# Kernel tuning notes

Measured on AMD Instinct MI355X. Metric: run time of the kernel, lower is better.

Reference implementation:

```python
import jax, jax.numpy as jnp
import numpy as np

ALPHA = 0.95
B, T, IN, HID, CTX, OUT = 64, 512, 256, 512, 256, 128
HORIZON = 1


def _scrn_layer(x, Wx, bx, Uc, Vh):
    # x: [B, T, D_in]; Wx: [CTX, D_in]; bx: [CTX]; Uc: [HID, CTX]; Vh: [HID, HID]
    # Input projection is time-parallel; only the recurrence is sequential.
    xp = jnp.einsum('btd,cd->btc', x, Wx) + bx  # [B, T, CTX]
    h0 = jnp.zeros((x.shape[0], Vh.shape[0]), dtype=x.dtype)
    c0 = jnp.zeros((x.shape[0], Wx.shape[0]), dtype=x.dtype)

    def step(carry, xp_t):
        h, c = carry
        c = (1.0 - ALPHA) * c + ALPHA * xp_t
        h = jnp.tanh(jnp.dot(c, Uc.T) + jnp.dot(h, Vh.T))
        return (h, c), h

    (_, _), hs = jax.lax.scan(step, (h0, c0), jnp.swapaxes(xp, 0, 1))
    return jnp.swapaxes(hs, 0, 1)  # [B, T, HID]


def setup_inputs() -> dict:
    key = jax.random.key(0)
    ks = jax.random.split(key, 12)

    def lin(k, fan_in, shape):
        bound = 1.0 / np.sqrt(fan_in)
        return jax.random.uniform(k, shape, jnp.float32, -bound, bound)

    return {
        'x': jax.random.normal(ks[0], (B, T, IN), jnp.float32),
        'Wx0': lin(ks[1], IN, (CTX, IN)),
        'bx0': lin(ks[2], IN, (CTX,)),
        'Uc0': lin(ks[3], CTX, (HID, CTX)),
        'Vh0': lin(ks[4], HID, (HID, HID)),
        'Wx1': lin(ks[5], HID, (CTX, HID)),
        'bx1': lin(ks[6], HID, (CTX,)),
        'Uc1': lin(ks[7], CTX, (HID, CTX)),
        'Vh1': lin(ks[8], HID, (HID, HID)),
        'fc_w': lin(ks[9], HID, (OUT, HID)),
        'fc_b': lin(ks[10], HID, (OUT,)),
    }


def reference(x, Wx0, bx0, Uc0, Vh0, Wx1, bx1, Uc1, Vh1, fc_w, fc_b):
    out = _scrn_layer(x, Wx0, bx0, Uc0, Vh0)
    out = _scrn_layer(out, Wx1, bx1, Uc1, Vh1)
    out = out[:, -HORIZON:, :]  # [B, HORIZON, HID]
    return jnp.einsum('bth,oh->bto', out, fc_w) + fc_b  # [B, HORIZON, OUT]
```

## Files before the change

kernel.cpp:

```cpp
#include <hip/hip_runtime.h>


typedef _Float16 f16;
typedef _Float16 f16x8 __attribute__((ext_vector_type(8)));
typedef _Float16 f16x2 __attribute__((ext_vector_type(2)));
typedef float f32x4 __attribute__((ext_vector_type(4)));
typedef unsigned short u16;
typedef unsigned int u32;
typedef unsigned short u16x8 __attribute__((ext_vector_type(8)));
typedef unsigned long long u64;

#define DEV __device__ __forceinline__

constexpr int Tt = 512, HIDq = 512;
constexpr int RS = 32;
constexpr int DSd = 32;

DEV float bf2f(u16 u) { unsigned v = ((unsigned)u) << 16; float f; __builtin_memcpy(&f, &v, 4); return f; }
DEV u16 f2bf(float f) { unsigned u; __builtin_memcpy(&u, &f, 4); u = (u + 0x7fffu + ((u >> 16) & 1u)) >> 16; return (u16)u; }
DEV float fast_tanh(float x) {
  x = fminf(30.f, fmaxf(-30.f, x));
  float e = exp2f(x * 2.885390081777927f);
  return (e - 1.f) / (e + 1.f);
}
DEV u64 al64(const u64* p) { return __hip_atomic_load(p, __ATOMIC_RELAXED, __HIP_MEMORY_SCOPE_AGENT); }
DEV u32 al32(const u32* p) { return __hip_atomic_load(p, __ATOMIC_RELAXED, __HIP_MEMORY_SCOPE_AGENT); }
DEV void as32(u32* p, u32 v) { __hip_atomic_store(p, v, __ATOMIC_RELAXED, __HIP_MEMORY_SCOPE_AGENT); }

__global__ void k_probe(const u16* __restrict__ w, int* __restrict__ dmode) {
  __shared__ int s;
  if (threadIdx.x == 0) s = 0;
  __syncthreads();
  int found = 0;
  for (int i = threadIdx.x; i < 8192; i += 256) {
    float v = bf2f(w[i]);
    if (fabsf(v) > 0.5f) found = 1;
  }
  if (found) atomicOr(&s, 1);
  __syncthreads();
  if (threadIdx.x == 0) *dmode = s;
}

__global__ void k_cvt(const void* __restrict__ src, f16* __restrict__ dst, int n8,
                      const int* __restrict__ dmode) {
  int i = blockIdx.x * 256 + threadIdx.x;
  if (i >= n8) return;
  f16x8 o;
  if (*dmode) {
    const float4* s = (const float4*)src;
    float4 a = s[2*i], b = s[2*i+1];
    o[0]=(f16)a.x; o[1]=(f16)a.y; o[2]=(f16)a.z; o[3]=(f16)a.w;
    o[4]=(f16)b.x; o[5]=(f16)b.y; o[6]=(f16)b.z; o[7]=(f16)b.w;
  } else {
    u16x8 v = ((const u16x8*)src)[i];
#pragma unroll
    for (int j = 0; j < 8; ++j) o[j] = (f16)bf2f(v[j]);
  }
  ((f16x8*)dst)[i] = o;
}

__global__ void k_zero(u16* __restrict__ out) {
  out[blockIdx.x * 256 + threadIdx.x] = 0;
}

__global__ __launch_bounds__(256) void k_tr(const f16* __restrict__ src, f16* __restrict__ dst,
                                            int R, int cshift) {
  int idx = blockIdx.x * 256 + threadIdx.x;
  int r = idx >> cshift, c = idx & ((1 << cshift) - 1);
  dst[c * R + r] = src[idx];
}

__global__ __launch_bounds__(512) void k_bias(const f16* __restrict__ Uc, const f16* __restrict__ bx,
                                              f16* __restrict__ out) {
  int j = threadIdx.x;
  float a = 0.f;
  for (int c = 0; c < 256; ++c) a += (float)Uc[j * 256 + c] * (float)bx[c];
  out[j] = (f16)a;
}

__global__ __launch_bounds__(128) void k_ema(const f16* __restrict__ xp, f16* __restrict__ c) {
  int b = blockIdx.x >> 3, chunk = blockIdx.x & 7;
  int t0 = chunk * 64;
  int ch = threadIdx.x;
  const f16x2* src = (const f16x2*)(xp + (size_t)b * Tt * 256) + ch;
  f16x2* dst = (f16x2*)(c + (size_t)b * Tt * 256) + ch;
  float c0 = 0.f, c1 = 0.f;
  int ts = (t0 >= 16) ? t0 - 16 : 0;
  for (int tt = ts; tt < t0 + 64; ++tt) {
    f16x2 v = src[(size_t)tt * 128];
    c0 = 0.05f * c0 + 0.95f * (float)v.x;
    c1 = 0.05f * c1 + 0.95f * (float)v.y;
    if (tt >= t0) { f16x2 o; o.x = (f16)c0; o.y = (f16)c1; dst[(size_t)tt * 128] = o; }
  }
}

template<bool HAS_BIAS, bool TD>
__global__ __launch_bounds__(256) void k_gemm(const f16* __restrict__ A, const f16* __restrict__ Bm,
                                              const f16* __restrict__ bias, f16* __restrict__ C,
                                              int M, int N, int K) {
  __shared__ f16 As[128][40];
  __shared__ f16 Bs[128][40];
  const int tid = threadIdx.x, lane = tid & 63, wv = tid >> 6;
  const int l15 = lane & 15, q = lane >> 4;
  const int wm = wv >> 1, wn = wv & 1;
  const int m0 = blockIdx.y * 128, n0 = blockIdx.x * 128;
  const int srow = tid >> 1, sseg = tid & 1;
  f32x4 acc[4][4] = {};
  const f16* ga = A  + (size_t)(m0 + srow) * K + sseg * 16;
  const f16* gb = Bm + (size_t)(n0 + srow) * K + sseg * 16;
  for (int k0 = 0; k0 < K; k0 += 32) {
    f16x8 a0 = *(const f16x8*)(ga + k0);
    f16x8 a1 = *(const f16x8*)(ga + k0 + 8);
    f16x8 b0 = *(const f16x8*)(gb + k0);
    f16x8 b1 = *(const f16x8*)(gb + k0 + 8);
    __syncthreads();
    *(f16x8*)&As[srow][sseg*16]     = a0;
    *(f16x8*)&As[srow][sseg*16 + 8] = a1;
    *(f16x8*)&Bs[srow][sseg*16]     = b0;
    *(f16x8*)&Bs[srow][sseg*16 + 8] = b1;
    __syncthreads();
    f16x8 af[4], bf[4];
#pragma unroll
    for (int i = 0; i < 4; ++i) af[i] = *(const f16x8*)&As[wm*64 + i*16 + l15][q*8];
#pragma unroll
    for (int i = 0; i < 4; ++i) bf[i] = *(const f16x8*)&Bs[wn*64 + i*16 + l15][q*8];
#pragma unroll
    for (int i = 0; i < 4; ++i)
#pragma unroll
      for (int j = 0; j < 4; ++j)
        acc[i][j] = __builtin_amdgcn_mfma_f32_16x16x32_f16(af[i], bf[j], acc[i][j], 0, 0, 0);
  }
#pragma unroll
  for (int j = 0; j < 4; ++j) {
    int col = n0 + wn*64 + j*16 + l15;
    float bv = HAS_BIAS ? (float)bias[col] : 0.f;
#pragma unroll
    for (int i = 0; i < 4; ++i)
#pragma unroll
      for (int r = 0; r < 4; ++r) {
        int row = m0 + wm*64 + i*16 + q*4 + r;
        size_t orow = TD ? (size_t)((row & 511) * 64 + (row >> 9)) : (size_t)row;
        C[orow * N + col] = (f16)(acc[i][j][r] + bv);
      }
  }
}

__global__ __launch_bounds__(512, 2) void k_mega(const f16* __restrict__ Vh0,
                                                 const f16* __restrict__ Vh1,
                                                 const f16* __restrict__ W2,
                                                 const f16* __restrict__ b2,
                                                 const f16* __restrict__ d1,
                                                 u32* __restrict__ ring,
                                                 u32* __restrict__ d2r,
                                                 u32* __restrict__ hb1,
                                                 u32* __restrict__ hb2,
                                                 u32* __restrict__ prog,
                                                 u32* __restrict__ eprog) {
  __shared__ f16 hL[2][16][520];
  const int bb = blockIdx.x;
  const int tid = threadIdx.x, w = tid >> 6, lane = tid & 63;
  const int l15 = lane & 15, q = lane >> 4;

  if (bb < 8) {
    const int hf = bb & 1, g = bb >> 1;
    const int colbase = 256*hf + 32*w;
    f16x8 Bf[2][16];
#pragma unroll
    for (int j = 0; j < 2; ++j)
#pragma unroll
      for (int kk = 0; kk < 16; ++kk)
        Bf[j][kk] = *(const f16x8*)&Vh0[(size_t)(colbase + 16*j + l15) * HIDq + kk*32 + q*8];
    for (int i = tid; i < 1024; i += 512) {
      int r = i >> 6, c = (i & 63) * 8;
      f16x8 z = {};
      *(f16x8*)&hL[0][r][c] = z;
    }
    float dv[2][4];
#pragma unroll
    for (int j = 0; j < 2; ++j)
#pragma unroll
      for (int r = 0; r < 4; ++r)
        dv[j][r] = (float)d1[(size_t)(16*g + q*4 + r) * HIDq + colbase + 16*j + l15];
    __syncthreads();
    const int irow = tid >> 5, ic8 = (tid & 31) * 8;
    const int pcol = 256*(hf ^ 1) + ic8;
    int eprog_c = 0;

    for (int t = 0; t < Tt; ++t) {
      const int rb = t & 1, wb = rb ^ 1, slot = t & 1;
      f32x4 a00 = {}, a01 = {}, a10 = {}, a11 = {};
#pragma unroll
      for (int kk = 0; kk < 16; ++kk) {
        f16x8 a = *(const f16x8*)&hL[rb][l15][kk*32 + q*8];
        if (kk & 1) {
          a01 = __builtin_amdgcn_mfma_f32_16x16x32_f16(a, Bf[0][kk], a01, 0, 0, 0);
          a11 = __builtin_amdgcn_mfma_f32_16x16x32_f16(a, Bf[1][kk], a11, 0, 0, 0);
        } else {
          a00 = __builtin_amdgcn_mfma_f32_16x16x32_f16(a, Bf[0][kk], a00, 0, 0, 0);
          a10 = __builtin_amdgcn_mfma_f32_16x16x32_f16(a, Bf[1][kk], a10, 0, 0, 0);
        }
      }
      const u32 tagw = (u32)(t + 1) << 16;
      u32* rslot = ring + (size_t)(t & (RS - 1)) * 32768;
      u16 hbits[2][4];
#pragma unroll
      for (int j = 0; j < 2; ++j) {
        f32x4 s = j ? (a10 + a11) : (a00 + a01);
#pragma unroll
        for (int r = 0; r < 4; ++r) {
          float z = s[r] + dv[j][r];
          union { f16 h; u16 u; } cv; cv.h = (f16)fast_tanh(z);
          hbits[j][r] = cv.u;
          as32(&hb1[(size_t)slot * 32768 + (size_t)(16*g + q*4 + r) * HIDq + colbase + 16*j + l15],
               tagw | (u32)cv.u);
        }
      }
#pragma unroll
      for (int j = 0; j < 2; ++j)
#pragma unroll
        for (int r = 0; r < 4; ++r)
          as32(&rslot[(size_t)(16*g + q*4 + r) * HIDq + colbase + 16*j + l15],
               tagw | (u32)hbits[j][r]);
#pragma unroll
      for (int j = 0; j < 2; ++j)
#pragma unroll
        for (int r = 0; r < 4; ++r) {
          union { u16 u; f16 h; } cv; cv.u = hbits[j][r];
          hL[wb][q*4 + r][colbase + 16*j + l15] = cv.h;
        }
      if (t < Tt - 1) {
#pragma unroll
        for (int j = 0; j < 2; ++j)
#pragma unroll
          for (int r = 0; r < 4; ++r)
            dv[j][r] = (float)d1[((size_t)(t+1)*64 + 16*g + q*4 + r) * HIDq + colbase + 16*j + l15];
      }
      if (tid == 0 && eprog_c < t - 30) {
        const u64* ep = (const u64*)&eprog[2 * g];
        for (;;) {
          u64 e2 = al64(ep);
          int lo = (int)(u32)e2, hi = (int)(u32)(e2 >> 32);
          eprog_c = lo < hi ? lo : hi;
          if (eprog_c >= t - 30) break;
          __builtin_amdgcn_s_sleep(1);
        }
      }
      {
        const u64* pp = (const u64*)(hb1 + (size_t)slot * 32768 + (size_t)(16*g + irow) * HIDq)
                      + (pcol >> 1);
        u64 v[4];
#pragma unroll
        for (int jj = 0; jj < 4; ++jj) v[jj] = al64(pp + jj);
        for (;;) {
          u32 bad = 0;
#pragma unroll
          for (int jj = 0; jj < 4; ++jj)
            bad |= ((u32)v[jj] ^ tagw) | ((u32)(v[jj] >> 32) ^ tagw);
          if ((bad & 0xFFFF0000u) == 0) break;
          __builtin_amdgcn_s_sleep(1);
#pragma unroll
          for (int jj = 0; jj < 4; ++jj) v[jj] = al64(pp + jj);
        }
        union { u32 wd[4]; f16x8 vv; } fr;
#pragma unroll
        for (int jj = 0; jj < 4; ++jj)
          fr.wd[jj] = __builtin_amdgcn_perm((u32)(v[jj] >> 32), (u32)v[jj], 0x05040100u);
        *(f16x8*)&hL[wb][irow][pcol] = fr.vv;
      }
      __syncthreads();
    }

  } else if (bb < 16) {
    const int eb = bb - 8, hf = eb & 1, g = eb >> 1;
    const int colbase = 256*hf + 32*w;
    f16x8 Bf[2][16];
#pragma unroll
    for (int j = 0; j < 2; ++j)
#pragma unroll
      for (int kk = 0; kk < 16; ++kk)
        Bf[j][kk] = *(const f16x8*)&W2[(size_t)(colbase + 16*j + l15) * HIDq + kk*32 + q*8];
    float bv[2] = { (float)b2[colbase + l15], (float)b2[colbase + 16 + l15] };
    float ed[2][4] = {};
    const int irow = tid >> 5, icol = (tid & 31) * 16;
    int sprog_c = 0;

    for (int t = 0; t < Tt; ++t) {
      if (tid == 0) {
        if (t > 0) as32(&eprog[eb], (u32)t);
        if (sprog_c < t - 32) {
          for (;;) {
            sprog_c = (int)al32(&prog[eb]);
            if (sprog_c >= t - 32) break;
            __builtin_amdgcn_s_sleep(1);
          }
        }
      }
      const u32 tagw = (u32)(t + 1) << 16;
      {
        const u64* pp = (const u64*)(ring + (size_t)(t & (RS - 1)) * 32768
                          + (size_t)(16*g + irow) * HIDq) + (icol >> 1);
        u64 v[8];
#pragma unroll
        for (int jj = 0; jj < 8; ++jj) v[jj] = al64(pp + jj);
        for (;;) {
          u32 bad = 0;
#pragma unroll
          for (int jj = 0; jj < 8; ++jj)
            bad |= ((u32)v[jj] ^ tagw) | ((u32)(v[jj] >> 32) ^ tagw);
          if ((bad & 0xFFFF0000u) == 0) break;
          __builtin_amdgcn_s_sleep(1);
#pragma unroll
          for (int jj = 0; jj < 8; ++jj) v[jj] = al64(pp + jj);
        }
        union { u32 wd[8]; f16x8 vv[2]; } fr;
#pragma unroll
        for (int jj = 0; jj < 8; ++jj)
          fr.wd[jj] = __builtin_amdgcn_perm((u32)(v[jj] >> 32), (u32)v[jj], 0x05040100u);
        *(f16x8*)&hL[t & 1][irow][icol]     = fr.vv[0];
        *(f16x8*)&hL[t & 1][irow][icol + 8] = fr.vv[1];
      }
      __syncthreads();
      f32x4 a00 = {}, a01 = {}, a10 = {}, a11 = {};
#pragma unroll
      for (int kk = 0; kk < 16; ++kk) {
        f16x8 a = *(const f16x8*)&hL[t & 1][l15][kk*32 + q*8];
        if (kk & 1) {
          a01 = __builtin_amdgcn_mfma_f32_16x16x32_f16(a, Bf[0][kk], a01, 0, 0, 0);
          a11 = __builtin_amdgcn_mfma_f32_16x16x32_f16(a, Bf[1][kk], a11, 0, 0, 0);
        } else {
          a00 = __builtin_amdgcn_mfma_f32_16x16x32_f16(a, Bf[0][kk], a00, 0, 0, 0);
          a10 = __builtin_amdgcn_mfma_f32_16x16x32_f16(a, Bf[1][kk], a10, 0, 0, 0);
        }
      }
      u32* dslot = d2r + (size_t)(t & (DSd - 1)) * 32768;
#pragma unroll
      for (int j = 0; j < 2; ++j) {
        f32x4 s = j ? (a10 + a11) : (a00 + a01);
#pragma unroll
        for (int r = 0; r < 4; ++r) {
          ed[j][r] = 0.05f * ed[j][r] + 0.95f * (s[r] + bv[j]);
          union { f16 h; u16 u; } cv; cv.h = (f16)ed[j][r];
          as32(&dslot[(size_t)(16*g + q*4 + r) * HIDq + colbase + 16*j + l15],
               tagw | (u32)cv.u);
        }
      }
    }

  } else {
    const int sb = bb - 16, hf = sb & 1, g = sb >> 1;
    const int colbase = 256*hf + 32*w;
    f16x8 Bf[2][16];
#pragma unroll
    for (int j = 0; j < 2; ++j)
#pragma unroll
      for (int kk = 0; kk < 16; ++kk)
        Bf[j][kk] = *(const f16x8*)&Vh1[(size_t)(colbase + 16*j + l15) * HIDq + kk*32 + q*8];
    for (int i = tid; i < 1024; i += 512) {
      int r = i >> 6, c = (i & 63) * 8;
      f16x8 z = {};
      *(f16x8*)&hL[0][r][c] = z;
    }
    float dv[2][4];
    {
      const u32 tag2 = 1u << 16;
      const u32* dp = d2r + (size_t)(16*g + q*4) * HIDq + colbase + l15;
      u32 vv[8];
      for (;;) {
#pragma unroll
        for (int i = 0; i < 8; ++i) vv[i] = al32(dp + (size_t)(i & 3) * HIDq + 16*(i >> 2));
        u32 bad = 0;
#pragma unroll
        for (int i = 0; i < 8; ++i) bad |= vv[i] ^ tag2;
        if ((bad & 0xFFFF0000u) == 0) break;
        __builtin_amdgcn_s_sleep(1);
      }
#pragma unroll
      for (int j = 0; j < 2; ++j)
#pragma unroll
        for (int r = 0; r < 4; ++r) {
          union { u16 u; f16 h; } cv; cv.u = (u16)vv[j*4 + r];
          dv[j][r] = (float)cv.h;
        }
    }
    __syncthreads();
    const int irow = tid >> 5, ic8 = (tid & 31) * 8;
    const int pcol = 256*(hf ^ 1) + ic8;

    for (int t = 0; t < Tt; ++t) {
      const int rb = t & 1, wb = rb ^ 1, slot = t & 1;
      if (tid == 0 && t > 0) as32(&prog[sb], (u32)t);
      f32x4 a00 = {}, a01 = {}, a10 = {}, a11 = {};
#pragma unroll
      for (int kk = 0; kk < 16; ++kk) {
        f16x8 a = *(const f16x8*)&hL[rb][l15][kk*32 + q*8];
        if (kk & 1) {
          a01 = __builtin_amdgcn_mfma_f32_16x16x32_f16(a, Bf[0][kk], a01, 0, 0, 0);
          a11 = __builtin_amdgcn_mfma_f32_16x16x32_f16(a, Bf[1][kk], a11, 0, 0, 0);
        } else {
          a00 = __builtin_amdgcn_mfma_f32_16x16x32_f16(a, Bf[0][kk], a00, 0, 0, 0);
          a10 = __builtin_amdgcn_mfma_f32_16x16x32_f16(a, Bf[1][kk], a10, 0, 0, 0);
        }
      }
      const u32 tagw = (u32)(t + 1) << 16;
      u16 hbits[2][4];
#pragma unroll
      for (int j = 0; j < 2; ++j) {
        f32x4 s = j ? (a10 + a11) : (a00 + a01);
#pragma unroll
        for (int r = 0; r < 4; ++r) {
          float z = s[r] + dv[j][r];
          union { f16 h; u16 u; } cv; cv.h = (f16)fast_tanh(z);
          hbits[j][r] = cv.u;
          as32(&hb2[(size_t)(slot*64 + 16*g + q*4 + r) * HIDq + colbase + 16*j + l15],
               tagw | (u32)cv.u);
        }
      }
#pragma unroll
      for (int j = 0; j < 2; ++j)
#pragma unroll
        for (int r = 0; r < 4; ++r) {
          union { u16 u; f16 h; } cv; cv.u = hbits[j][r];
          hL[wb][q*4 + r][colbase + 16*j + l15] = cv.h;
        }

      {
        const bool have_d = (t < Tt - 1);
        const u32 tag2 = (u32)(t + 2) << 16;
        const u32* dp = d2r + (size_t)((t + 1) & (DSd - 1)) * 32768
                      + (size_t)(16*g + q*4) * HIDq + colbase + l15;
        const u64* pp = (const u64*)&hb2[(size_t)(slot*64 + 16*g + irow) * HIDq] + (pcol >> 1);
        u32 vv[8];
        u64 v[4];
        if (have_d) {
#pragma unroll
          for (int i = 0; i < 8; ++i) vv[i] = al32(dp + (size_t)(i & 3) * HIDq + 16*(i >> 2));
        }
#pragma unroll
        for (int jj = 0; jj < 4; ++jj) v[jj] = al64(pp + jj);
        for (;;) {
          u32 badp = 0;
#pragma unroll
          for (int jj = 0; jj < 4; ++jj)
            badp |= ((u32)v[jj] ^ tagw) | ((u32)(v[jj] >> 32) ^ tagw);
          badp &= 0xFFFF0000u;
          u32 badd = 0;
          if (have_d) {
#pragma unroll
            for (int i = 0; i < 8; ++i) badd |= vv[i] ^ tag2;
            badd &= 0xFFFF0000u;
          }
          if (!(badp | badd)) break;
          __builtin_amdgcn_s_sleep(1);
          if (badp) {
#pragma unroll
            for (int jj = 0; jj < 4; ++jj) v[jj] = al64(pp + jj);
          }
          if (badd) {
#pragma unroll
            for (int i = 0; i < 8; ++i) vv[i] = al32(dp + (size_t)(i & 3) * HIDq + 16*(i >> 2));
          }
        }
        if (have_d) {
#pragma unroll
          for (int j = 0; j < 2; ++j)
#pragma unroll
            for (int r = 0; r < 4; ++r) {
              union { u16 u; f16 h; } cv; cv.u = (u16)vv[j*4 + r];
              dv[j][r] = (float)cv.h;
            }
        }
        union { u32 wd[4]; f16x8 vr; } fr;
#pragma unroll
        for (int jj = 0; jj < 4; ++jj)
          fr.wd[jj] = __builtin_amdgcn_perm((u32)(v[jj] >> 32), (u32)v[jj], 0x05040100u);
        *(f16x8*)&hL[wb][irow][pcol] = fr.vr;
      }
      __syncthreads();
    }
  }
}

__global__ __launch_bounds__(64) void k_final(const u32* __restrict__ h, const f16* __restrict__ fw,
                                              const f16* __restrict__ fb, void* __restrict__ outv,
                                              const int* __restrict__ dmode) {
  __shared__ f16 hA[16][520];
  __shared__ f16 Bw[16][520];
  const int mb = blockIdx.x & 3, nb = blockIdx.x >> 2;
  const int lane = threadIdx.x, l15 = lane & 15, q = lane >> 4;
  for (int i = lane; i < 16 * 128; i += 64) {
    int r = i >> 7, c = (i & 127) * 4;
    const u64* p = (const u64*)&h[(size_t)(mb*16 + r) * 512 + c];
    u64 v0 = al64(p), v1 = al64(p + 1);
    *(u32*)&hA[r][c]     = __builtin_amdgcn_perm((u32)(v0 >> 32), (u32)v0, 0x05040100u);
    *(u32*)&hA[r][c + 2] = __builtin_amdgcn_perm((u32)(v1 >> 32), (u32)v1, 0x05040100u);
  }
  for (int i = lane; i < 16 * 64; i += 64) {
    int r = i >> 6, c = (i & 63) * 8;
    *(f16x8*)&Bw[r][c] = *(const f16x8*)&fw[(size_t)(nb*16 + r) * 512 + c];
  }
  __syncthreads();
  f32x4 acc = {};
#pragma unroll
  for (int kk = 0; kk < 16; ++kk) {
    f16x8 a = *(const f16x8*)&hA[l15][kk*32 + q*8];
    f16x8 b = *(const f16x8*)&Bw[l15][kk*32 + q*8];
    acc = __builtin_amdgcn_mfma_f32_16x16x32_f16(a, b, acc, 0, 0, 0);
  }
  float bv = (float)fb[nb*16 + l15];
  int md = *dmode;
#pragma unroll
  for (int r = 0; r < 4; ++r) {
    int idx = (mb*16 + q*4 + r) * 128 + nb*16 + l15;
    float val = acc[r] + bv;
    if (md) ((float*)outv)[idx] = val;
    else    ((u16*)outv)[idx]   = f2bf(val);
  }
}

extern "C" void kernel_launch(void* const* d_in, const int* in_sizes, int n_in,
                              void* d_out, int out_size, void* d_ws, size_t ws_size,
                              hipStream_t stream) {
  if (ws_size < 88080384ull) {
    k_zero<<<32, 256, 0, stream>>>((u16*)d_out);
    return;
  }
  char* ws = (char*)d_ws;
  u32* hb2   = (u32*)(ws + 0);
  u32* hb1   = (u32*)(ws + 262144);
  u32* prog  = (u32*)(ws + 524288);
  u32* eprog = (u32*)(ws + 524320);
  int* dmode = (int*)(ws + 524352);
  f16* Wx0f = (f16*)(ws + 1048576);
  f16* Uc0f = (f16*)(ws + 1179648);
  f16* Vh0f = (f16*)(ws + 1441792);
  f16* Wx1f = (f16*)(ws + 1966080);
  f16* Uc1f = (f16*)(ws + 2228224);
  f16* Vh1f = (f16*)(ws + 2490368);
  f16* fcwf = (f16*)(ws + 3014656);
  f16* bx0f = (f16*)(ws + 3145728);
  f16* bx1f = (f16*)(ws + 3146240);
  f16* fcbf = (f16*)(ws + 3146752);
  f16* Wx1T = (f16*)(ws + 3147776);
  f16* W2f  = (f16*)(ws + 3409920);
  f16* b2f  = (f16*)(ws + 3934208);
  f16* x16  = (f16*)(ws + 4194304);
  u32* ring = (u32*)(ws + 4194304);
  f16* xp1  = (f16*)(ws + 20971520);
  f16* cb1  = (f16*)(ws + 37748736);
  u32* d2r  = (u32*)(ws + 37748736);
  f16* d1   = (f16*)(ws + 54525952);

  hipMemsetAsync(ws, 0, 524352, stream);
  k_probe<<<1, 256, 0, stream>>>((const u16*)d_in[1], dmode);
  auto cvt = [&](const void* s, f16* d, int n) {
    int n8 = n / 8;
    k_cvt<<<dim3((n8 + 255) / 256), dim3(256), 0, stream>>>(s, d, n8, dmode);
  };
  cvt(d_in[0],  x16,  8388608);
  cvt(d_in[1],  Wx0f, 65536);
  cvt(d_in[2],  bx0f, 256);
  cvt(d_in[3],  Uc0f, 131072);
  cvt(d_in[4],  Vh0f, 262144);
  cvt(d_in[5],  Wx1f, 131072);
  cvt(d_in[6],  bx1f, 256);
  cvt(d_in[7],  Uc1f, 131072);
  cvt(d_in[8],  Vh1f, 262144);
  cvt(d_in[9],  fcwf, 65536);
  cvt(d_in[10], fcbf, 128);

  k_tr<<<512, 256, 0, stream>>>(Wx1f, Wx1T, 256, 9);
  k_bias<<<1, 512, 0, stream>>>(Uc1f, bx1f, b2f);
  k_gemm<false, false><<<dim3(4, 4), 256, 0, stream>>>(Uc1f, Wx1T, nullptr, W2f, 512, 512, 256);

  k_gemm<true , false><<<dim3(2, 256), 256, 0, stream>>>(x16, Wx0f, bx0f, xp1, 32768, 256, 256);
  k_ema<<<512, 128, 0, stream>>>(xp1, cb1);
  hipMemsetAsync(ws + 4194304, 0, 4194304, stream);
  k_gemm<false, true ><<<dim3(4, 256), 256, 0, stream>>>(cb1, Uc0f, nullptr, d1, 32768, 512, 256);
  hipMemsetAsync(ws + 37748736, 0, 4194304, stream);

  k_mega<<<24, 512, 0, stream>>>(Vh0f, Vh1f, W2f, b2f, d1, ring, d2r, hb1, hb2, prog, eprog);

  k_final<<<32, 64, 0, stream>>>(hb2 + 64 * 512, fcwf, fcbf, d_out, dmode);
}
```

Before: 1.833 ms.

## Add per-block progress counters to gate ring polling and reorder ring stores

Moves the layer-1 ring writes after the critical peer-exchange read so the recurrence's inter-block handoff runs first. Adds progress counters (s1p, d2p) that layer-1 and middle blocks publish, so consumers spin on one counter instead of repeatedly polling large tagged buffers. It also lengthens sleep intervals in the spin loops. The aim is to cut memory traffic from polling and shorten the critical path, at the cost of an extra block-wide barrier and extra atomic stores per step.

New measurement: 2.015 ms. 10.0% more time.

```diff
diff --git a/kernel.cpp b/kernel.cpp
--- a/kernel.cpp
+++ b/kernel.cpp
@@ -155,7 +155,9 @@
                                                  u32* __restrict__ hb1,
                                                  u32* __restrict__ hb2,
                                                  u32* __restrict__ prog,
-                                                 u32* __restrict__ eprog) {
+                                                 u32* __restrict__ eprog,
+                                                 u32* __restrict__ s1p,
+                                                 u32* __restrict__ d2p) {
   __shared__ f16 hL[2][16][520];
   const int bb = blockIdx.x;
   const int tid = threadIdx.x, w = tid >> 6, lane = tid & 63;
@@ -201,7 +203,6 @@
         }
       }
       const u32 tagw = (u32)(t + 1) << 16;
-      u32* rslot = ring + (size_t)(t & (RS - 1)) * 32768;
       u16 hbits[2][4];
 #pragma unroll
       for (int j = 0; j < 2; ++j) {
@@ -218,12 +219,6 @@
 #pragma unroll
       for (int j = 0; j < 2; ++j)
 #pragma unroll
-        for (int r = 0; r < 4; ++r)
-          as32(&rslot[(size_t)(16*g + q*4 + r) * HIDq + colbase + 16*j + l15],
-               tagw | (u32)hbits[j][r]);
-#pragma unroll
-      for (int j = 0; j < 2; ++j)
-#pragma unroll
         for (int r = 0; r < 4; ++r) {
           union { u16 u; f16 h; } cv; cv.u = hbits[j][r];
           hL[wb][q*4 + r][colbase + 16*j + l15] = cv.h;
@@ -234,16 +229,6 @@
 #pragma unroll
           for (int r = 0; r < 4; ++r)
             dv[j][r] = (float)d1[((size_t)(t+1)*64 + 16*g + q*4 + r) * HIDq + colbase + 16*j + l15];
-      }
-      if (tid == 0 && eprog_c < t - 30) {
-        const u64* ep = (const u64*)&eprog[2 * g];
-        for (;;) {
-          u64 e2 = al64(ep);
-          int lo = (int)(u32)e2, hi = (int)(u32)(e2 >> 32);
-          eprog_c = lo < hi ? lo : hi;
-          if (eprog_c >= t - 30) break;
-          __builtin_amdgcn_s_sleep(1);
-        }
       }
       {
         const u64* pp = (const u64*)(hb1 + (size_t)slot * 32768 + (size_t)(16*g + irow) * HIDq)
@@ -266,6 +251,28 @@
         for (int jj = 0; jj < 4; ++jj)
           fr.wd[jj] = __builtin_amdgcn_perm((u32)(v[jj] >> 32), (u32)v[jj], 0x05040100u);
         *(f16x8*)&hL[wb][irow][pcol] = fr.vv;
+      }
+      {
+        u32* rslot = ring + (size_t)(t & (RS - 1)) * 32768;
+#pragma unroll
+        for (int j = 0; j < 2; ++j)
+#pragma unroll
+          for (int r = 0; r < 4; ++r)
+            as32(&rslot[(size_t)(16*g + q*4 + r) * HIDq + colbase + 16*j + l15],
+                 tagw | (u32)hbits[j][r]);
+      }
+      if (tid == 0) {
+        as32(&s1p[bb], (u32)(t + 1));
+        if (eprog_c < t - 30) {
+          const u64* ep = (const u64*)&eprog[2 * g];
+          for (;;) {
+            u64 e2 = al64(ep);
+            int lo = (int)(u32)e2, hi = (int)(u32)(e2 >> 32);
+            eprog_c = lo < hi ? lo : hi;
+            if (eprog_c >= t - 30) break;
+            __builtin_amdgcn_s_sleep(2);
+          }
+        }
       }
       __syncthreads();
     }
@@ -291,10 +298,21 @@
           for (;;) {
             sprog_c = (int)al32(&prog[eb]);
             if (sprog_c >= t - 32) break;
-            __builtin_amdgcn_s_sleep(1);
+            __builtin_amdgcn_s_sleep(2);
           }
         }
-      }
+        {
+          const u64* sp = (const u64*)&s1p[2 * g];
+          for (;;) {
+            u64 s2 = al64(sp);
+            int lo = (int)(u32)s2, hi = (int)(u32)(s2 >> 32);
+            int mn = lo < hi ? lo : hi;
+            if (mn >= t + 1) break;
+            __builtin_amdgcn_s_sleep(2);
+          }
+        }
+      }
+      __syncthreads();
       const u32 tagw = (u32)(t + 1) << 16;
       {
         const u64* pp = (const u64*)(ring + (size_t)(t & (RS - 1)) * 32768
@@ -344,6 +362,7 @@
                tagw | (u32)cv.u);
         }
       }
+      if (tid == 0) as32(&d2p[eb], (u32)(t + 1));
     }
 
   } else {
@@ -372,7 +391,8 @@
 #pragma unroll
         for (int i = 0; i < 8; ++i) bad |= vv[i] ^ tag2;
         if ((bad & 0xFFFF0000u) == 0) break;
-        __builtin_amdgcn_s_sleep(1);
+        __builtin_amdgcn_s_sleep(2);
+        while ((int)al32(&d2p[sb]) < 1) __builtin_amdgcn_s_sleep(2);
       }
 #pragma unroll
       for (int j = 0; j < 2; ++j)
@@ -456,8 +476,10 @@
             for (int jj = 0; jj < 4; ++jj) v[jj] = al64(pp + jj);
           }
           if (badd) {
-#pragma unroll
-            for (int i = 0; i < 8; ++i) vv[i] = al32(dp + (size_t)(i & 3) * HIDq + 16*(i >> 2));
+            if ((int)al32(&d2p[sb]) >= (int)(t + 2)) {
+#pragma unroll
+              for (int i = 0; i < 8; ++i) vv[i] = al32(dp + (size_t)(i & 3) * HIDq + 16*(i >> 2));
+            }
           }
         }
         if (have_d) {
@@ -530,6 +552,8 @@
   u32* prog  = (u32*)(ws + 524288);
   u32* eprog = (u32*)(ws + 524320);
   int* dmode = (int*)(ws + 524352);
+  u32* s1p   = (u32*)(ws + 524384);
+  u32* d2p   = (u32*)(ws + 524416);
   f16* Wx0f = (f16*)(ws + 1048576);
   f16* Uc0f = (f16*)(ws + 1179648);
   f16* Vh0f = (f16*)(ws + 1441792);
@@ -550,7 +574,7 @@
   u32* d2r  = (u32*)(ws + 37748736);
   f16* d1   = (f16*)(ws + 54525952);
 
-  hipMemsetAsync(ws, 0, 524352, stream);
+  hipMemsetAsync(ws, 0, 524448, stream);
   k_probe<<<1, 256, 0, stream>>>((const u16*)d_in[1], dmode);
   auto cvt = [&](const void* s, f16* d, int n) {
     int n8 = n / 8;
@@ -578,7 +602,8 @@
   k_gemm<false, true ><<<dim3(4, 256), 256, 0, stream>>>(cb1, Uc0f, nullptr, d1, 32768, 512, 256);
   hipMemsetAsync(ws + 37748736, 0, 4194304, stream);
 
-  k_mega<<<24, 512, 0, stream>>>(Vh0f, Vh1f, W2f, b2f, d1, ring, d2r, hb1, hb2, prog, eprog);
+  k_mega<<<24, 512, 0, stream>>>(Vh0f, Vh1f, W2f, b2f, d1, ring, d2r, hb1, hb2,
+                                 prog, eprog, s1p, d2p);
 
   k_final<<<32, 64, 0, stream>>>(hb2 + 64 * 512, fcwf, fcbf, d_out, dmode);
 }
```
